# Performance work log

Measured on AMD Instinct MI355X. Metric: run time of the kernel, lower is better.

Reference implementation:

```python
import jax, jax.numpy as jnp
import numpy as np

NUM_ITER = 3
SLOT_DIM = 16
INPUT_DIM = 256
HIDDEN_DIM = 128
EPS = 1e-8
LN_EPS = 1e-5  # torch LayerNorm default


def _layernorm(x, w, b):
    mu = jnp.mean(x, axis=-1, keepdims=True)
    var = jnp.mean((x - mu) ** 2, axis=-1, keepdims=True)
    return (x - mu) * jax.lax.rsqrt(var + LN_EPS) * w + b


def setup_inputs() -> dict:
    key = jax.random.key(0)
    ks = jax.random.split(key, 12)
    B, N, K = 32, 4096, 8
    D, S, H = INPUT_DIM, SLOT_DIM, HIDDEN_DIM
    inputs = jax.random.normal(ks[0], (B, N, D), dtype=jnp.float32)
    init_slots = jax.random.normal(ks[1], (B, K, S), dtype=jnp.float32)
    return {
        "inputs": inputs,
        "init_slots": init_slots,
        "ln_in_w": jnp.ones((D,), jnp.float32),
        "ln_in_b": jnp.zeros((D,), jnp.float32),
        "ln_s_w": jnp.ones((S,), jnp.float32),
        "ln_s_b": jnp.zeros((S,), jnp.float32),
        "ln_m_w": jnp.ones((S,), jnp.float32),
        "ln_m_b": jnp.zeros((S,), jnp.float32),
        "wq": jax.random.normal(ks[2], (S, S), jnp.float32) * (S ** -0.5),
        "wk": jax.random.normal(ks[3], (S, D), jnp.float32) * (D ** -0.5),
        "wv": jax.random.normal(ks[4], (S, D), jnp.float32) * (D ** -0.5),
        "w_ih": jax.random.normal(ks[5], (3 * S, S), jnp.float32) * (S ** -0.5),
        "w_hh": jax.random.normal(ks[6], (3 * S, S), jnp.float32) * (S ** -0.5),
        "b_ih": jnp.zeros((3 * S,), jnp.float32),
        "b_hh": jnp.zeros((3 * S,), jnp.float32),
        "mlp_w1": jax.random.normal(ks[7], (H, S), jnp.float32) * (S ** -0.5),
        "mlp_b1": jnp.zeros((H,), jnp.float32),
        "mlp_w2": jax.random.normal(ks[8], (S, H), jnp.float32) * (H ** -0.5),
        "mlp_b2": jnp.zeros((S,), jnp.float32),
    }


def _gru_cell(x, h, w_ih, w_hh, b_ih, b_hh):
    # torch GRUCell: gates ordered [r, z, n]
    gi = x @ w_ih.T + b_ih            # [BK, 3S]
    gh = h @ w_hh.T + b_hh
    i_r, i_z, i_n = jnp.split(gi, 3, axis=-1)
    h_r, h_z, h_n = jnp.split(gh, 3, axis=-1)
    r = jax.nn.sigmoid(i_r + h_r)
    z = jax.nn.sigmoid(i_z + h_z)
    n = jnp.tanh(i_n + r * h_n)
    return (1.0 - z) * n + z * h


def reference(inputs, init_slots, ln_in_w, ln_in_b, ln_s_w, ln_s_b, ln_m_w, ln_m_b,
              wq, wk, wv, w_ih, w_hh, b_ih, b_hh, mlp_w1, mlp_b1, mlp_w2, mlp_b2):
    B, N, _ = inputs.shape
    K = init_slots.shape[1]
    scale = SLOT_DIM ** -0.5

    x = _layernorm(inputs, ln_in_w, ln_in_b)
    k = jnp.einsum('bnd,sd->bns', x, wk)   # [B,N,S]
    v = jnp.einsum('bnd,sd->bns', x, wv)

    slots = init_slots
    attn = None
    for _ in range(NUM_ITER):
        slots_prev = slots
        q = jnp.einsum('bks,ts->bkt', _layernorm(slots, ln_s_w, ln_s_b), wq)
        logits = jnp.einsum('bks,bns->bkn', q, k) * scale       # [B,K,N]
        attn = jax.nn.softmax(logits, axis=1) + EPS              # softmax over SLOTS
        attn = attn / jnp.sum(attn, axis=-1, keepdims=True)
        updates = jnp.einsum('bkn,bns->bks', attn, v)            # [B,K,S]
        h = _gru_cell(updates.reshape(B * K, -1), slots_prev.reshape(B * K, -1),
                      w_ih, w_hh, b_ih, b_hh).reshape(B, K, -1)
        y = _layernorm(h, ln_m_w, ln_m_b)
        mlp = jax.nn.relu(y @ mlp_w1.T + mlp_b1) @ mlp_w2.T + mlp_b2
        slots = h + mlp
    return slots, attn
```

## Files before the change

### kernel.cpp

```cpp
#include <hip/hip_runtime.h>
#include <cstddef>


typedef unsigned short ushort_t;
typedef __attribute__((ext_vector_type(8))) short short8;
typedef __attribute__((ext_vector_type(4))) float f32x4;

__device__ __forceinline__ float sigmoid_f(float x){ return 1.f/(1.f+__expf(-x)); }
__device__ __forceinline__ float tanh_f(float x){ return 1.f - 2.f/(__expf(2.f*x)+1.f); }

__device__ __forceinline__ ushort_t f2bf(float x){
  unsigned u = __float_as_uint(x);
  return (ushort_t)((u + 0x7FFFu + ((u>>16)&1u)) >> 16);
}
__device__ __forceinline__ float bf2f(ushort_t b){
  return __uint_as_float(((unsigned)b) << 16);
}
__device__ __forceinline__ void split_bf(float v, short& hi, short& lo){
  unsigned u = __float_as_uint(v);
  hi = (short)(u >> 16);
  float hf = __uint_as_float(u & 0xFFFF0000u);
  lo = (short)(__float_as_uint(v - hf) >> 16);
}

__global__ __launch_bounds__(256) void k_prep(
    const float* __restrict__ lnw, const float* __restrict__ lnb,
    const float* __restrict__ wk, const float* __restrict__ wv,
    const float* __restrict__ init_slots,
    const float* __restrict__ ln_s_w, const float* __restrict__ ln_s_b,
    const float* __restrict__ wq,
    ushort_t* __restrict__ Wh, ushort_t* __restrict__ Wl,
    float* __restrict__ mt,
    float* __restrict__ qbuf, float* __restrict__ upd, float* __restrict__ Abuf,
    float* __restrict__ slots_out)
{
  int t = threadIdx.x;
  int i = blockIdx.x*256 + t;
  {
    int s = i >> 8, d = i & 255;
    float w = (s < 16) ? wk[s*256+d] : wv[(s-16)*256+d];
    float w0 = lnw[d]*w;
    ushort_t hb = f2bf(w0);
    ushort_t lb = f2bf(w0 - bf2f(hb));
    Wh[i] = hb; Wl[i] = lb;
  }
  if (blockIdx.x != 0) return;
  {
    int s = t >> 3, j = t & 7;
    float m = 0.f, tv = 0.f;
    for (int d = j; d < 256; d += 8) {
      float w = (s < 16) ? wk[s*256+d] : wv[(s-16)*256+d];
      float w0 = lnw[d]*w;
      ushort_t hb = f2bf(w0);
      float hf = bf2f(hb);
      float lf = bf2f(f2bf(w0 - hf));
      m  += hf + lf;
      tv  = fmaf(lnb[d], w, tv);
    }
    m += __shfl_xor(m,1);  m += __shfl_xor(m,2);  m += __shfl_xor(m,4);
    tv += __shfl_xor(tv,1); tv += __shfl_xor(tv,2); tv += __shfl_xor(tv,4);
    if (j == 0) { mt[s] = m; mt[32+s] = tv; }
  }
  #pragma unroll
  for (int j2 = 0; j2 < 16; ++j2) {
    slots_out[t*16+j2] = init_slots[t*16+j2];
    upd[t*16+j2] = 0.f;
  }
  Abuf[t] = 0.f;
  float sl[16];
  #pragma unroll
  for (int j2 = 0; j2 < 16; ++j2) sl[j2] = init_slots[t*16+j2];
  float mu = 0.f;
  #pragma unroll
  for (int j2 = 0; j2 < 16; ++j2) mu += sl[j2];
  mu *= (1.f/16.f);
  float var = 0.f;
  #pragma unroll
  for (int j2 = 0; j2 < 16; ++j2) { float d = sl[j2]-mu; var = fmaf(d,d,var); }
  var *= (1.f/16.f);
  float rstd = rsqrtf(var + 1e-5f);
  float y[16];
  #pragma unroll
  for (int j2 = 0; j2 < 16; ++j2) y[j2] = (sl[j2]-mu)*rstd*ln_s_w[j2] + ln_s_b[j2];
  #pragma unroll
  for (int tq = 0; tq < 16; ++tq) {
    float q = 0.f;
    #pragma unroll
    for (int s2 = 0; s2 < 16; ++s2) q = fmaf(y[s2], wq[tq*16+s2], q);
    qbuf[t*16+tq] = q;
  }
}

__global__ __launch_bounds__(256, 4) void k_proj(
    const float* __restrict__ x, const ushort_t* __restrict__ Wh,
    const ushort_t* __restrict__ Wl, const float* __restrict__ mt,
    float* __restrict__ kout, float* __restrict__ vout)
{
  __shared__ ushort_t wlds[64*264];
  int t = threadIdx.x;
  int lane = t & 63;
  int p = __builtin_amdgcn_readfirstlane(t >> 6);
  int m = lane & 15, quad = lane >> 4;
  int r0 = blockIdx.x*64;

  {
    const unsigned* srcH = (const unsigned*)Wh;
    const unsigned* srcL = (const unsigned*)Wl;
    unsigned* dst = (unsigned*)wlds;
    #pragma unroll
    for (int i0 = 0; i0 < 8192; i0 += 256) {
      int i = i0 + t;
      int r = i >> 7, w = i & 127;
      unsigned v = (r < 32) ? srcH[r*128 + w] : srcL[(r-32)*128 + w];
      dst[r*132 + w] = v;
    }
  }
  __syncthreads();

  const ushort_t* rhk = wlds + (size_t)m*264 + quad*8;
  const ushort_t* rhv = wlds + (size_t)(16+m)*264 + quad*8;
  const ushort_t* rlk = wlds + (size_t)(32+m)*264 + quad*8;
  const ushort_t* rlv = wlds + (size_t)(48+m)*264 + quad*8;

  const float* xr = x + (size_t)(r0 + p*16 + m)*256 + quad*8;

  f32x4 acck = {0.f,0.f,0.f,0.f}, accv = {0.f,0.f,0.f,0.f};
  float sum = 0.f, sumsq = 0.f;

  #pragma unroll
  for (int kk = 0; kk < 8; ++kk) {
    float4 a0 = *(const float4*)(xr + kk*32);
    float4 a1 = *(const float4*)(xr + kk*32 + 4);
    short8 bh_k = *(const short8*)(rhk + kk*32);
    short8 bh_v = *(const short8*)(rhv + kk*32);
    short8 bl_k = *(const short8*)(rlk + kk*32);
    short8 bl_v = *(const short8*)(rlv + kk*32);
    float xv[8] = {a0.x,a0.y,a0.z,a0.w, a1.x,a1.y,a1.z,a1.w};
    short8 ah, al;
    #pragma unroll
    for (int j = 0; j < 8; ++j) {
      float v = xv[j];
      sum += v; sumsq = fmaf(v, v, sumsq);
      short h_, l_;
      split_bf(v, h_, l_);
      ah[j] = h_; al[j] = l_;
    }
    acck = __builtin_amdgcn_mfma_f32_16x16x32_bf16(ah, bh_k, acck, 0, 0, 0);
    accv = __builtin_amdgcn_mfma_f32_16x16x32_bf16(ah, bh_v, accv, 0, 0, 0);
    acck = __builtin_amdgcn_mfma_f32_16x16x32_bf16(al, bh_k, acck, 0, 0, 0);
    accv = __builtin_amdgcn_mfma_f32_16x16x32_bf16(al, bh_v, accv, 0, 0, 0);
    acck = __builtin_amdgcn_mfma_f32_16x16x32_bf16(ah, bl_k, acck, 0, 0, 0);
    accv = __builtin_amdgcn_mfma_f32_16x16x32_bf16(ah, bl_v, accv, 0, 0, 0);
  }

  sum   += __shfl_xor(sum, 16);  sum   += __shfl_xor(sum, 32);
  sumsq += __shfl_xor(sumsq, 16); sumsq += __shfl_xor(sumsq, 32);

  float mtk  = mt[m],    mtv  = mt[16+m];
  float mtkb = mt[32+m], mtvb = mt[48+m];
  #pragma unroll
  for (int r = 0; r < 4; ++r) {
    int row = quad*4 + r;
    float s_ = __shfl(sum,   row);
    float q_ = __shfl(sumsq, row);
    float mu = s_*(1.f/256.f);
    float var = q_*(1.f/256.f) - mu*mu;
    float rstd = rsqrtf(var + 1e-5f);
    float ok = fmaf(rstd, acck[r] - mu*mtk, mtkb);
    float ov = fmaf(rstd, accv[r] - mu*mtv, mtvb);
    size_t grow = (size_t)(r0 + p*16 + row)*16 + m;
    kout[grow] = ok;
    vout[grow] = ov;
  }
}

__global__ __launch_bounds__(256) void k_attn(
    const float* __restrict__ kproj, const float* __restrict__ vproj,
    const float* __restrict__ qbuf,
    float* __restrict__ upd, float* __restrict__ Abuf,
    float* __restrict__ attn_out, int write_attn)
{
  __shared__ ushort_t vt[32*264];
  __shared__ ushort_t pt[32*264];
  __shared__ float qs[128];
  __shared__ float apart[4][8];
  int b = blockIdx.x >> 4;
  int n0 = (blockIdx.x & 15) * 256;
  int t = threadIdx.x;
  int w = t >> 6, lane = t & 63;

  if (t < 128) qs[t] = qbuf[b*128 + t];

  const float* kr = kproj + ((size_t)(b*4096 + n0 + t))*16;
  const float* vr = vproj + ((size_t)(b*4096 + n0 + t))*16;
  float kv[16], vv[16];
  #pragma unroll
  for (int j = 0; j < 16; j += 4) {
    float4 f = *(const float4*)(kr+j);
    kv[j]=f.x; kv[j+1]=f.y; kv[j+2]=f.z; kv[j+3]=f.w;
    float4 g = *(const float4*)(vr+j);
    vv[j]=g.x; vv[j+1]=g.y; vv[j+2]=g.z; vv[j+3]=g.w;
  }
  #pragma unroll
  for (int s = 0; s < 16; ++s) {
    short h_, l_;
    split_bf(vv[s], h_, l_);
    vt[s*264 + t] = (ushort_t)h_;
    vt[(16+s)*264 + t] = (ushort_t)l_;
  }
  __syncthreads();

  float p8[8];
  {
    float lg[8];
    #pragma unroll
    for (int kk = 0; kk < 8; ++kk) {
      float a = 0.f;
      #pragma unroll
      for (int s = 0; s < 16; ++s) a = fmaf(qs[kk*16+s], kv[s], a);
      lg[kk] = a*0.25f;
    }
    float mx = lg[0];
    #pragma unroll
    for (int kk = 1; kk < 8; ++kk) mx = fmaxf(mx, lg[kk]);
    float se = 0.f;
    #pragma unroll
    for (int kk = 0; kk < 8; ++kk) { lg[kk] = __expf(lg[kk]-mx); se += lg[kk]; }
    float inv = 1.f/se;
    #pragma unroll
    for (int kk = 0; kk < 8; ++kk) {
      float pv = fmaf(lg[kk], inv, 1e-8f);
      p8[kk] = pv;
      if (write_attn) attn_out[((size_t)(b*8+kk))*4096 + n0 + t] = pv;
    }
  }
  #pragma unroll
  for (int kk = 0; kk < 8; ++kk) {
    float r = p8[kk];
    r += __shfl_xor(r, 1);  r += __shfl_xor(r, 2);  r += __shfl_xor(r, 4);
    r += __shfl_xor(r, 8);  r += __shfl_xor(r, 16); r += __shfl_xor(r, 32);
    if (lane == 0) apart[w][kk] = r;
  }
  #pragma unroll
  for (int kk = 0; kk < 8; ++kk) {
    short h_, l_;
    split_bf(p8[kk], h_, l_);
    pt[kk*264 + t] = (ushort_t)h_;
    pt[(16+kk)*264 + t] = (ushort_t)l_;
  }
  __syncthreads();

  if (t < 8)
    atomicAdd(Abuf + b*8 + t,
              apart[0][t] + apart[1][t] + apart[2][t] + apart[3][t]);

  if (w == 0) {
    int mm = lane & 15, quad = lane >> 4;
    const short8 z8 = {0,0,0,0,0,0,0,0};
    f32x4 acc = {0.f,0.f,0.f,0.f};
    #pragma unroll
    for (int c = 0; c < 8; ++c) {
      int k0 = c*32 + quad*8;
      short8 ah = (mm < 8) ? *(const short8*)&pt[mm*264 + k0]      : z8;
      short8 al = (mm < 8) ? *(const short8*)&pt[(16+mm)*264 + k0] : z8;
      short8 bh = *(const short8*)&vt[mm*264 + k0];
      short8 bl = *(const short8*)&vt[(16+mm)*264 + k0];
      acc = __builtin_amdgcn_mfma_f32_16x16x32_bf16(ah, bh, acc, 0, 0, 0);
      acc = __builtin_amdgcn_mfma_f32_16x16x32_bf16(al, bh, acc, 0, 0, 0);
      acc = __builtin_amdgcn_mfma_f32_16x16x32_bf16(ah, bl, acc, 0, 0, 0);
    }
    int s = lane & 15;
    #pragma unroll
    for (int r = 0; r < 4; ++r) {
      int kk = quad*4 + r;
      if (kk < 8) atomicAdd(upd + (b*8+kk)*16 + s, acc[r]);
    }
  }
}

__device__ __forceinline__ void gru_body(
    int bk, int s, int laneBase, int prep_next,
    float* upd, float* Abuf, float* slots, float* qbuf,
    const float* s_wih, const float* s_whh,
    const float* s_bih, const float* s_bhh,
    const float* s_w1, const float* s_b1,
    const float* s_w2, const float* s_b2,
    const float* s_lnmw, const float* s_lnmb,
    const float* s_lnsw, const float* s_lnsb, const float* s_wq)
{
  float inv = 1.f / Abuf[bk];
  float u[16], h[16];
  #pragma unroll
  for (int j = 0; j < 16; ++j) {
    u[j] = upd[bk*16+j] * inv;
    h[j] = slots[bk*16+j];
  }
  float hs = slots[bk*16+s];

  float gir = s_bih[s],  giz = s_bih[16+s], gin = s_bih[32+s];
  float ghr = s_bhh[s],  ghz = s_bhh[16+s], ghn = s_bhh[32+s];
  #pragma unroll
  for (int j = 0; j < 16; ++j) {
    gir = fmaf(u[j], s_wih[s*17+j], gir);
    giz = fmaf(u[j], s_wih[(16+s)*17+j], giz);
    gin = fmaf(u[j], s_wih[(32+s)*17+j], gin);
    ghr = fmaf(h[j], s_whh[s*17+j], ghr);
    ghz = fmaf(h[j], s_whh[(16+s)*17+j], ghz);
    ghn = fmaf(h[j], s_whh[(32+s)*17+j], ghn);
  }
  float rr = sigmoid_f(gir + ghr);
  float zz = sigmoid_f(giz + ghz);
  float nn = tanh_f(gin + rr*ghn);
  float hn = (1.f-zz)*nn + zz*hs;

  float ssum = hn;
  #pragma unroll
  for (int mm = 1; mm < 16; mm <<= 1) ssum += __shfl_xor(ssum, mm);
  float mu = ssum*(1.f/16.f);
  float dv = hn - mu;
  float vs = dv*dv;
  #pragma unroll
  for (int mm = 1; mm < 16; mm <<= 1) vs += __shfl_xor(vs, mm);
  float rstd = rsqrtf(vs*(1.f/16.f) + 1e-5f);
  float y = dv*rstd*s_lnmw[s] + s_lnmb[s];

  float yv[16];
  #pragma unroll
  for (int j = 0; j < 16; ++j) yv[j] = __shfl(y, laneBase + j);

  float h1[8];
  #pragma unroll
  for (int i = 0; i < 8; ++i) {
    int jj = i*16 + s;
    float a = s_b1[jj];
    #pragma unroll
    for (int q = 0; q < 16; ++q) a = fmaf(yv[q], s_w1[jj*17+q], a);
    h1[i] = fmaxf(a, 0.f);
  }
  float o = s_b2[s];
  #pragma unroll
  for (int i = 0; i < 8; ++i) {
    #pragma unroll
    for (int sp = 0; sp < 16; ++sp) {
      float hv = __shfl(h1[i], laneBase + sp);
      o = fmaf(hv, s_w2[s*129 + i*16 + sp], o);
    }
  }
  float slot_new = hn + o;
  slots[bk*16+s] = slot_new;

  if (prep_next) {
    float ss = slot_new;
    #pragma unroll
    for (int mm = 1; mm < 16; mm <<= 1) ss += __shfl_xor(ss, mm);
    float mu2 = ss*(1.f/16.f);
    float d2 = slot_new - mu2;
    float v2 = d2*d2;
    #pragma unroll
    for (int mm = 1; mm < 16; mm <<= 1) v2 += __shfl_xor(v2, mm);
    float rstd2 = rsqrtf(v2*(1.f/16.f) + 1e-5f);
    float y2 = d2*rstd2*s_lnsw[s] + s_lnsb[s];
    float qv = 0.f;
    #pragma unroll
    for (int sp = 0; sp < 16; ++sp)
      qv = fmaf(__shfl(y2, laneBase+sp), s_wq[s*17+sp], qv);
    qbuf[bk*16+s] = qv;
    upd[bk*16+s] = 0.f;
    if (s == 0) Abuf[bk] = 0.f;
  }
}

#define GRU_STAGE_LDS()                                                      \
  __shared__ float s_wih[48*17], s_whh[48*17];                               \
  __shared__ float s_bih[48], s_bhh[48];                                     \
  __shared__ float s_w1[128*17], s_b1[128];                                  \
  __shared__ float s_w2[16*129], s_b2[16];                                   \
  __shared__ float s_lnmw[16], s_lnmb[16], s_lnsw[16], s_lnsb[16];           \
  __shared__ float s_wq[16*17];                                              \
  {                                                                          \
    int t_ = threadIdx.x;                                                    \
    for (int i = t_; i < 768; i += 256) {                                    \
      int g = i >> 4, j = i & 15;                                            \
      s_wih[g*17+j] = w_ih[i];                                               \
      s_whh[g*17+j] = w_hh[i];                                               \
    }                                                                        \
    for (int i = t_; i < 2048; i += 256) {                                   \
      int r = i >> 4, c = i & 15;                                            \
      s_w1[r*17+c] = mlp_w1[i];                                              \
      int r2 = i >> 7, c2 = i & 127;                                         \
      s_w2[r2*129+c2] = mlp_w2[i];                                           \
    }                                                                        \
    if (t_ < 48) { s_bih[t_] = b_ih[t_]; s_bhh[t_] = b_hh[t_]; }             \
    if (t_ < 128) s_b1[t_] = mlp_b1[t_];                                     \
    if (t_ < 16) {                                                           \
      s_b2[t_] = mlp_b2[t_];                                                 \
      s_lnmw[t_] = ln_m_w[t_]; s_lnmb[t_] = ln_m_b[t_];                      \
      s_lnsw[t_] = ln_s_w[t_]; s_lnsb[t_] = ln_s_b[t_];                      \
    }                                                                        \
    for (int i = t_; i < 256; i += 256) {                                    \
      int r = i >> 4, c = i & 15;                                            \
      s_wq[r*17+c] = wq[i];                                                  \
    }                                                                        \
  }                                                                          \
  __syncthreads();

__global__ __launch_bounds__(256) void k_gru(
    float* __restrict__ upd, float* __restrict__ Abuf,
    float* __restrict__ slots, float* __restrict__ qbuf,
    const float* __restrict__ w_ih, const float* __restrict__ w_hh,
    const float* __restrict__ b_ih, const float* __restrict__ b_hh,
    const float* __restrict__ mlp_w1, const float* __restrict__ mlp_b1,
    const float* __restrict__ mlp_w2, const float* __restrict__ mlp_b2,
    const float* __restrict__ ln_m_w, const float* __restrict__ ln_m_b,
    const float* __restrict__ ln_s_w, const float* __restrict__ ln_s_b,
    const float* __restrict__ wq)
{
  GRU_STAGE_LDS()
  int t = threadIdx.x;
  int bk = blockIdx.x*16 + (t >> 4);
  int s = t & 15;
  int laneBase = (t & 63) & ~15;
  gru_body(bk, s, laneBase, 1, upd, Abuf, slots, qbuf,
           s_wih, s_whh, s_bih, s_bhh, s_w1, s_b1, s_w2, s_b2,
           s_lnmw, s_lnmb, s_lnsw, s_lnsb, s_wq);
}

__global__ __launch_bounds__(256) void k_final(
    float* __restrict__ upd, float* __restrict__ Abuf,
    float* __restrict__ slots, float* __restrict__ qbuf,
    float* __restrict__ attn,
    const float* __restrict__ w_ih, const float* __restrict__ w_hh,
    const float* __restrict__ b_ih, const float* __restrict__ b_hh,
    const float* __restrict__ mlp_w1, const float* __restrict__ mlp_b1,
    const float* __restrict__ mlp_w2, const float* __restrict__ mlp_b2,
    const float* __restrict__ ln_m_w, const float* __restrict__ ln_m_b,
    const float* __restrict__ ln_s_w, const float* __restrict__ ln_s_b,
    const float* __restrict__ wq)
{
  int t = threadIdx.x;
  {
    int bk = blockIdx.x;
    float inv = 1.f / Abuf[bk];
    float4* p = (float4*)(attn + (size_t)bk*4096);
    #pragma unroll 4
    for (int i = t; i < 1024; i += 256) {
      float4 v = p[i];
      v.x *= inv; v.y *= inv; v.z *= inv; v.w *= inv;
      p[i] = v;
    }
  }
  if (blockIdx.x >= 16) return;
  GRU_STAGE_LDS()
  int bk = blockIdx.x*16 + (t >> 4);
  int s = t & 15;
  int laneBase = (t & 63) & ~15;
  gru_body(bk, s, laneBase, 0, upd, Abuf, slots, qbuf,
           s_wih, s_whh, s_bih, s_bhh, s_w1, s_b1, s_w2, s_b2,
           s_lnmw, s_lnmb, s_lnsw, s_lnsb, s_wq);
}

extern "C" void kernel_launch(void* const* d_in, const int* in_sizes, int n_in,
                              void* d_out, int out_size, void* d_ws, size_t ws_size,
                              hipStream_t stream)
{
  const float* inputs     = (const float*)d_in[0];
  const float* init_slots = (const float*)d_in[1];
  const float* ln_in_w    = (const float*)d_in[2];
  const float* ln_in_b    = (const float*)d_in[3];
  const float* ln_s_w     = (const float*)d_in[4];
  const float* ln_s_b     = (const float*)d_in[5];
  const float* ln_m_w     = (const float*)d_in[6];
  const float* ln_m_b     = (const float*)d_in[7];
  const float* wq         = (const float*)d_in[8];
  const float* wk         = (const float*)d_in[9];
  const float* wv         = (const float*)d_in[10];
  const float* w_ih       = (const float*)d_in[11];
  const float* w_hh       = (const float*)d_in[12];
  const float* b_ih       = (const float*)d_in[13];
  const float* b_hh       = (const float*)d_in[14];
  const float* mlp_w1     = (const float*)d_in[15];
  const float* mlp_b1     = (const float*)d_in[16];
  const float* mlp_w2     = (const float*)d_in[17];
  const float* mlp_b2     = (const float*)d_in[18];

  float* ws    = (float*)d_ws;
  ushort_t* Wh = (ushort_t*)ws;
  ushort_t* Wl = (ushort_t*)(ws + 4096);
  float* mt    = ws + 8192;
  float* qbuf  = ws + 8320;
  float* upd   = ws + 12416;
  float* Abuf  = ws + 16512;
  float* kproj = ws + 16768;
  float* vproj = kproj + 2097152;

  float* out   = (float*)d_out;
  float* slots = out;
  float* attn  = out + 4096;

  k_prep<<<32, 256, 0, stream>>>(ln_in_w, ln_in_b, wk, wv, init_slots,
                                 ln_s_w, ln_s_b, wq,
                                 Wh, Wl, mt, qbuf, upd, Abuf, slots);
  k_proj<<<2048, 256, 0, stream>>>(inputs, Wh, Wl, mt, kproj, vproj);
  for (int it = 0; it < 3; ++it) {
    int last = (it == 2);
    k_attn<<<512, 256, 0, stream>>>(kproj, vproj, qbuf, upd, Abuf, attn, last);
    if (!last)
      k_gru<<<16, 256, 0, stream>>>(upd, Abuf, slots, qbuf,
                                    w_ih, w_hh, b_ih, b_hh,
                                    mlp_w1, mlp_b1, mlp_w2, mlp_b2,
                                    ln_m_w, ln_m_b, ln_s_w, ln_s_b, wq);
  }
  k_final<<<256, 256, 0, stream>>>(upd, Abuf, slots, qbuf, attn,
                                   w_ih, w_hh, b_ih, b_hh,
                                   mlp_w1, mlp_b1, mlp_w2, mlp_b2,
                                   ln_m_w, ln_m_b, ln_s_w, ln_s_b, wq);
}
```

Baseline: 287.2 us.

## Fuse projection, attention iterations and GRU into one cooperative kernel

```diff
diff --git a/kernel.cpp b/kernel.cpp
--- a/kernel.cpp
+++ b/kernel.cpp
@@ -1,5 +1,8 @@
 #include <hip/hip_runtime.h>
+#include <hip/hip_cooperative_groups.h>
 #include <cstddef>
+
+namespace cg = cooperative_groups;
 
 
 typedef unsigned short ushort_t;
@@ -62,11 +65,10 @@
     if (j == 0) { mt[s] = m; mt[32+s] = tv; }
   }
   #pragma unroll
-  for (int j2 = 0; j2 < 16; ++j2) {
+  for (int j2 = 0; j2 < 16; ++j2)
     slots_out[t*16+j2] = init_slots[t*16+j2];
-    upd[t*16+j2] = 0.f;
-  }
-  Abuf[t] = 0.f;
+  for (int i2 = t; i2 < 12288; i2 += 256) upd[i2] = 0.f;
+  for (int i2 = t; i2 < 768;   i2 += 256) Abuf[i2] = 0.f;
   float sl[16];
   #pragma unroll
   for (int j2 = 0; j2 < 16; ++j2) sl[j2] = init_slots[t*16+j2];
@@ -90,6 +92,337 @@
     qbuf[t*16+tq] = q;
   }
 }
+
+#define VT_OFF    0
+#define QS_OFF    16896
+#define SLOTS_OFF 17408
+#define APART_OFF 17920
+#define X_OFF     18048
+#define KLDS_OFF  (X_OFF + 33792)
+#define PT_OFF    X_OFF
+#define GW_OFF    (X_OFF + 8448)
+#define SMEM_BYTES 60544
+
+__global__ __launch_bounds__(256, 2) void k_mega(
+    const float* __restrict__ x,
+    const ushort_t* __restrict__ Wh, const ushort_t* __restrict__ Wl,
+    const float* __restrict__ mt, const float* __restrict__ qbuf,
+    const float* __restrict__ init_slots,
+    float* __restrict__ upd, float* __restrict__ Abuf,
+    float* __restrict__ slots_out, float* __restrict__ attn_out,
+    const float* __restrict__ w_ih, const float* __restrict__ w_hh,
+    const float* __restrict__ b_ih, const float* __restrict__ b_hh,
+    const float* __restrict__ mlp_w1, const float* __restrict__ mlp_b1,
+    const float* __restrict__ mlp_w2, const float* __restrict__ mlp_b2,
+    const float* __restrict__ ln_m_w, const float* __restrict__ ln_m_b,
+    const float* __restrict__ ln_s_w, const float* __restrict__ ln_s_b,
+    const float* __restrict__ wq)
+{
+  cg::grid_group grid = cg::this_grid();
+  __shared__ __align__(16) unsigned char smem[SMEM_BYTES];
+  ushort_t* vt     = (ushort_t*)(smem + VT_OFF);
+  float*    qs     = (float*)(smem + QS_OFF);
+  float*    sslots = (float*)(smem + SLOTS_OFF);
+  float*    apart  = (float*)(smem + APART_OFF);
+  ushort_t* wlds   = (ushort_t*)(smem + X_OFF);
+  float*    klds   = (float*)(smem + KLDS_OFF);
+  ushort_t* pt     = (ushort_t*)(smem + PT_OFF);
+  float*    s_wih  = (float*)(smem + GW_OFF);
+  float*    s_whh  = s_wih + 48*17;
+  float*    s_w1   = s_whh + 48*17;
+  float*    s_w2   = s_w1 + 128*17;
+  float*    s_bih  = s_w2 + 16*129;
+  float*    s_bhh  = s_bih + 48;
+  float*    s_b1   = s_bhh + 48;
+  float*    s_b2   = s_b1 + 128;
+  float*    s_lnmw = s_b2 + 16;
+  float*    s_lnmb = s_lnmw + 16;
+  float*    s_lnsw = s_lnmb + 16;
+  float*    s_lnsb = s_lnsw + 16;
+  float*    s_wq   = s_lnsb + 16;
+
+  int t = threadIdx.x;
+  int lane = t & 63;
+  int w = t >> 6;
+  int b  = blockIdx.x >> 4;
+  int nc = blockIdx.x & 15;
+  int n0 = nc << 8;
+
+  {
+    const unsigned* srcH = (const unsigned*)Wh;
+    const unsigned* srcL = (const unsigned*)Wl;
+    unsigned* dst = (unsigned*)wlds;
+    #pragma unroll
+    for (int i0 = 0; i0 < 8192; i0 += 256) {
+      int i = i0 + t;
+      int r = i >> 7, ww = i & 127;
+      unsigned v = (r < 32) ? srcH[r*128 + ww] : srcL[(r-32)*128 + ww];
+      dst[r*132 + ww] = v;
+    }
+  }
+  __syncthreads();
+
+  int m = lane & 15, quad = lane >> 4;
+  const ushort_t* rhk = wlds + (size_t)m*264 + quad*8;
+  const ushort_t* rhv = wlds + (size_t)(16+m)*264 + quad*8;
+  const ushort_t* rlk = wlds + (size_t)(32+m)*264 + quad*8;
+  const ushort_t* rlv = wlds + (size_t)(48+m)*264 + quad*8;
+  float mtk  = mt[m],    mtv  = mt[16+m];
+  float mtkb = mt[32+m], mtvb = mt[48+m];
+
+  float kv[16] = {0.f};
+  #pragma unroll
+  for (int half = 0; half < 2; ++half) {
+    #pragma unroll
+    for (int st = 0; st < 2; ++st) {
+      const float* xr = x + (size_t)(b*4096 + n0 + half*128 + st*64 + w*16 + m)*256
+                          + quad*8;
+      f32x4 acck = {0.f,0.f,0.f,0.f}, accv = {0.f,0.f,0.f,0.f};
+      float sum = 0.f, sumsq = 0.f;
+      #pragma unroll
+      for (int kk = 0; kk < 8; ++kk) {
+        float4 a0 = *(const float4*)(xr + kk*32);
+        float4 a1 = *(const float4*)(xr + kk*32 + 4);
+        short8 bh_k = *(const short8*)(rhk + kk*32);
+        short8 bh_v = *(const short8*)(rhv + kk*32);
+        short8 bl_k = *(const short8*)(rlk + kk*32);
+        short8 bl_v = *(const short8*)(rlv + kk*32);
+        float xv[8] = {a0.x,a0.y,a0.z,a0.w, a1.x,a1.y,a1.z,a1.w};
+        short8 ah, al;
+        #pragma unroll
+        for (int j = 0; j < 8; ++j) {
+          float v = xv[j];
+          sum += v; sumsq = fmaf(v, v, sumsq);
+          short h_, l_;
+          split_bf(v, h_, l_);
+          ah[j] = h_; al[j] = l_;
+        }
+        acck = __builtin_amdgcn_mfma_f32_16x16x32_bf16(ah, bh_k, acck, 0, 0, 0);
+        accv = __builtin_amdgcn_mfma_f32_16x16x32_bf16(ah, bh_v, accv, 0, 0, 0);
+        acck = __builtin_amdgcn_mfma_f32_16x16x32_bf16(al, bh_k, acck, 0, 0, 0);
+        accv = __builtin_amdgcn_mfma_f32_16x16x32_bf16(al, bh_v, accv, 0, 0, 0);
+        acck = __builtin_amdgcn_mfma_f32_16x16x32_bf16(ah, bl_k, acck, 0, 0, 0);
+        accv = __builtin_amdgcn_mfma_f32_16x16x32_bf16(ah, bl_v, accv, 0, 0, 0);
+      }
+      sum   += __shfl_xor(sum, 16);   sum   += __shfl_xor(sum, 32);
+      sumsq += __shfl_xor(sumsq, 16); sumsq += __shfl_xor(sumsq, 32);
+      #pragma unroll
+      for (int r = 0; r < 4; ++r) {
+        int row = quad*4 + r;
+        float s_ = __shfl(sum,   row);
+        float q_ = __shfl(sumsq, row);
+        float mu = s_*(1.f/256.f);
+        float var = q_*(1.f/256.f) - mu*mu;
+        float rstd = rsqrtf(var + 1e-5f);
+        float ok = fmaf(rstd, acck[r] - mu*mtk, mtkb);
+        float ov = fmaf(rstd, accv[r] - mu*mtv, mtvb);
+        int lr = st*64 + w*16 + row;
+        int rr = half*128 + lr;
+        klds[lr*17 + m] = ok;
+        short h_, l_;
+        split_bf(ov, h_, l_);
+        vt[m*264 + rr]      = (ushort_t)h_;
+        vt[(16+m)*264 + rr] = (ushort_t)l_;
+      }
+    }
+    __syncthreads();
+    if ((t >> 7) == half) {
+      int tl = t & 127;
+      #pragma unroll
+      for (int j = 0; j < 16; ++j) kv[j] = klds[tl*17 + j];
+    }
+    __syncthreads();
+  }
+
+  for (int i = t; i < 768; i += 256) {
+    int g = i >> 4, j = i & 15;
+    s_wih[g*17+j] = w_ih[i];
+    s_whh[g*17+j] = w_hh[i];
+  }
+  for (int i = t; i < 2048; i += 256) {
+    int r = i >> 4, c = i & 15;
+    s_w1[r*17+c] = mlp_w1[i];
+    int r2 = i >> 7, c2 = i & 127;
+    s_w2[r2*129+c2] = mlp_w2[i];
+  }
+  if (t < 48) { s_bih[t] = b_ih[t]; s_bhh[t] = b_hh[t]; }
+  if (t < 128) s_b1[t] = mlp_b1[t];
+  if (t < 16) {
+    s_b2[t] = mlp_b2[t];
+    s_lnmw[t] = ln_m_w[t]; s_lnmb[t] = ln_m_b[t];
+    s_lnsw[t] = ln_s_w[t]; s_lnsb[t] = ln_s_b[t];
+  }
+  for (int i = t; i < 256; i += 256) {
+    int r = i >> 4, c = i & 15;
+    s_wq[r*17+c] = wq[i];
+  }
+  if (t < 128) {
+    qs[t]     = qbuf[b*128 + t];
+    sslots[t] = init_slots[b*128 + t];
+  }
+  __syncthreads();
+
+  const short8 z8 = {0,0,0,0,0,0,0,0};
+  #pragma unroll 1
+  for (int it = 0; it < 3; ++it) {
+    float* upd_it = upd  + it*4096;
+    float* Ab_it  = Abuf + it*256;
+
+    float p8[8];
+    {
+      float lg[8];
+      #pragma unroll
+      for (int kk = 0; kk < 8; ++kk) {
+        float a = 0.f;
+        #pragma unroll
+        for (int s = 0; s < 16; ++s) a = fmaf(qs[kk*16+s], kv[s], a);
+        lg[kk] = a*0.25f;
+      }
+      float mx = lg[0];
+      #pragma unroll
+      for (int kk = 1; kk < 8; ++kk) mx = fmaxf(mx, lg[kk]);
+      float se = 0.f;
+      #pragma unroll
+      for (int kk = 0; kk < 8; ++kk) { lg[kk] = __expf(lg[kk]-mx); se += lg[kk]; }
+      float inv = 1.f/se;
+      #pragma unroll
+      for (int kk = 0; kk < 8; ++kk) p8[kk] = fmaf(lg[kk], inv, 1e-8f);
+    }
+    #pragma unroll
+    for (int kk = 0; kk < 8; ++kk) {
+      float r = p8[kk];
+      r += __shfl_xor(r, 1);  r += __shfl_xor(r, 2);  r += __shfl_xor(r, 4);
+      r += __shfl_xor(r, 8);  r += __shfl_xor(r, 16); r += __shfl_xor(r, 32);
+      if (lane == 0) apart[w*8 + kk] = r;
+    }
+    #pragma unroll
+    for (int kk = 0; kk < 8; ++kk) {
+      short h_, l_;
+      split_bf(p8[kk], h_, l_);
+      pt[kk*264 + t]     = (ushort_t)h_;
+      pt[(8+kk)*264 + t] = (ushort_t)l_;
+    }
+    __syncthreads();
+    if (t < 8)
+      atomicAdd(Ab_it + b*8 + t,
+                apart[t] + apart[8+t] + apart[16+t] + apart[24+t]);
+    if (w == 0) {
+      int mm = lane & 15, q2 = lane >> 4;
+      f32x4 acc = {0.f,0.f,0.f,0.f};
+      #pragma unroll
+      for (int c = 0; c < 8; ++c) {
+        int k0 = c*32 + q2*8;
+        short8 ah = (mm < 8) ? *(const short8*)&pt[mm*264 + k0]     : z8;
+        short8 al = (mm < 8) ? *(const short8*)&pt[(8+mm)*264 + k0] : z8;
+        short8 bh = *(const short8*)&vt[mm*264 + k0];
+        short8 bl = *(const short8*)&vt[(16+mm)*264 + k0];
+        acc = __builtin_amdgcn_mfma_f32_16x16x32_bf16(ah, bh, acc, 0, 0, 0);
+        acc = __builtin_amdgcn_mfma_f32_16x16x32_bf16(al, bh, acc, 0, 0, 0);
+        acc = __builtin_amdgcn_mfma_f32_16x16x32_bf16(ah, bl, acc, 0, 0, 0);
+      }
+      int s = lane & 15;
+      #pragma unroll
+      for (int r = 0; r < 4; ++r) {
+        int kk = q2*4 + r;
+        if (kk < 8) atomicAdd(upd_it + (b*8+kk)*16 + s, acc[r]);
+      }
+    }
+    __threadfence();
+    grid.sync();
+
+    if (it == 2) {
+      #pragma unroll
+      for (int kk = 0; kk < 8; ++kk) {
+        float inv = 1.f / Ab_it[b*8 + kk];
+        attn_out[((size_t)(b*8 + kk))*4096 + n0 + t] = p8[kk]*inv;
+      }
+    }
+    if (t < 128) {
+      int bk8 = t >> 4, s = t & 15;
+      int laneBase = (t & 63) & ~15;
+      float invA = 1.f / Ab_it[b*8 + bk8];
+      float u[16], h[16];
+      #pragma unroll
+      for (int j = 0; j < 16; ++j) {
+        u[j] = upd_it[(b*8 + bk8)*16 + j] * invA;
+        h[j] = sslots[bk8*16 + j];
+      }
+      float hs = h[s];
+      float gir = s_bih[s],  giz = s_bih[16+s], gin = s_bih[32+s];
+      float ghr = s_bhh[s],  ghz = s_bhh[16+s], ghn = s_bhh[32+s];
+      #pragma unroll
+      for (int j = 0; j < 16; ++j) {
+        gir = fmaf(u[j], s_wih[s*17+j], gir);
+        giz = fmaf(u[j], s_wih[(16+s)*17+j], giz);
+        gin = fmaf(u[j], s_wih[(32+s)*17+j], gin);
+        ghr = fmaf(h[j], s_whh[s*17+j], ghr);
+        ghz = fmaf(h[j], s_whh[(16+s)*17+j], ghz);
+        ghn = fmaf(h[j], s_whh[(32+s)*17+j], ghn);
+      }
+      float rr_ = sigmoid_f(gir + ghr);
+      float zz = sigmoid_f(giz + ghz);
+      float nn = tanh_f(gin + rr_*ghn);
+      float hn = (1.f - zz)*nn + zz*hs;
+
+      float ssum = hn;
+      #pragma unroll
+      for (int mm = 1; mm < 16; mm <<= 1) ssum += __shfl_xor(ssum, mm);
+      float mu = ssum*(1.f/16.f);
+      float dv = hn - mu;
+      float vs = dv*dv;
+      #pragma unroll
+      for (int mm = 1; mm < 16; mm <<= 1) vs += __shfl_xor(vs, mm);
+      float rstd = rsqrtf(vs*(1.f/16.f) + 1e-5f);
+      float y = dv*rstd*s_lnmw[s] + s_lnmb[s];
+
+      float yv[16];
+      #pragma unroll
+      for (int j = 0; j < 16; ++j) yv[j] = __shfl(y, laneBase + j);
+
+      float h1[8];
+      #pragma unroll
+      for (int i = 0; i < 8; ++i) {
+        int jj = i*16 + s;
+        float a = s_b1[jj];
+        #pragma unroll
+        for (int q = 0; q < 16; ++q) a = fmaf(yv[q], s_w1[jj*17+q], a);
+        h1[i] = fmaxf(a, 0.f);
+      }
+      float o = s_b2[s];
+      #pragma unroll
+      for (int i = 0; i < 8; ++i) {
+        #pragma unroll
+        for (int sp = 0; sp < 16; ++sp) {
+          float hv = __shfl(h1[i], laneBase + sp);
+          o = fmaf(hv, s_w2[s*129 + i*16 + sp], o);
+        }
+      }
+      float slot_new = hn + o;
+      if (it < 2) {
+        sslots[bk8*16 + s] = slot_new;
+        float ss = slot_new;
+        #pragma unroll
+        for (int mm = 1; mm < 16; mm <<= 1) ss += __shfl_xor(ss, mm);
+        float mu2 = ss*(1.f/16.f);
+        float d2 = slot_new - mu2;
+        float v2 = d2*d2;
+        #pragma unroll
+        for (int mm = 1; mm < 16; mm <<= 1) v2 += __shfl_xor(v2, mm);
+        float rstd2 = rsqrtf(v2*(1.f/16.f) + 1e-5f);
+        float y2 = d2*rstd2*s_lnsw[s] + s_lnsb[s];
+        float qv = 0.f;
+        #pragma unroll
+        for (int sp = 0; sp < 16; ++sp)
+          qv = fmaf(__shfl(y2, laneBase + sp), s_wq[s*17+sp], qv);
+        qs[bk8*16 + s] = qv;
+      } else if (nc == 0) {
+        slots_out[(b*8 + bk8)*16 + s] = slot_new;
+      }
+    }
+    __syncthreads();
+  }
+}
+
 
 __global__ __launch_bounds__(256, 4) void k_proj(
     const float* __restrict__ x, const ushort_t* __restrict__ Wh,
@@ -102,7 +435,6 @@
   int p = __builtin_amdgcn_readfirstlane(t >> 6);
   int m = lane & 15, quad = lane >> 4;
   int r0 = blockIdx.x*64;
-
   {
     const unsigned* srcH = (const unsigned*)Wh;
     const unsigned* srcL = (const unsigned*)Wl;
@@ -489,8 +821,8 @@
   float* mt    = ws + 8192;
   float* qbuf  = ws + 8320;
   float* upd   = ws + 12416;
-  float* Abuf  = ws + 16512;
-  float* kproj = ws + 16768;
+  float* Abuf  = ws + 24704;
+  float* kproj = ws + 25472;
   float* vproj = kproj + 2097152;
 
   float* out   = (float*)d_out;
@@ -500,6 +832,22 @@
   k_prep<<<32, 256, 0, stream>>>(ln_in_w, ln_in_b, wk, wv, init_slots,
                                  ln_s_w, ln_s_b, wq,
                                  Wh, Wl, mt, qbuf, upd, Abuf, slots);
+
+  {
+    void* kargs[] = {
+      (void*)&inputs, (void*)&Wh, (void*)&Wl, (void*)&mt, (void*)&qbuf,
+      (void*)&init_slots, (void*)&upd, (void*)&Abuf, (void*)&slots,
+      (void*)&attn, (void*)&w_ih, (void*)&w_hh, (void*)&b_ih, (void*)&b_hh,
+      (void*)&mlp_w1, (void*)&mlp_b1, (void*)&mlp_w2, (void*)&mlp_b2,
+      (void*)&ln_m_w, (void*)&ln_m_b, (void*)&ln_s_w, (void*)&ln_s_b,
+      (void*)&wq };
+    hipError_t err = hipLaunchCooperativeKernel((const void*)k_mega,
+                                                dim3(512), dim3(256),
+                                                kargs, 0, stream);
+    if (err == hipSuccess) return;
+    (void)hipGetLastError();
+  }
+
   k_proj<<<2048, 256, 0, stream>>>(inputs, Wh, Wl, mt, kproj, vproj);
   for (int it = 0; it < 3; ++it) {
     int last = (it == 2);
```

New measurement: 563.0 us. 96.1% more time.

## Store V pre-split to bf16 hi/lo planes transposed in projection kernel

Applied to the files above, without the earlier changes.

```diff
diff --git a/kernel.cpp b/kernel.cpp
--- a/kernel.cpp
+++ b/kernel.cpp
@@ -5,6 +5,8 @@
 typedef unsigned short ushort_t;
 typedef __attribute__((ext_vector_type(8))) short short8;
 typedef __attribute__((ext_vector_type(4))) float f32x4;
+
+#define VT_PLANE 2097152
 
 __device__ __forceinline__ float sigmoid_f(float x){ return 1.f/(1.f+__expf(-x)); }
 __device__ __forceinline__ float tanh_f(float x){ return 1.f - 2.f/(__expf(2.f*x)+1.f); }
@@ -94,15 +96,15 @@
 __global__ __launch_bounds__(256, 4) void k_proj(
     const float* __restrict__ x, const ushort_t* __restrict__ Wh,
     const ushort_t* __restrict__ Wl, const float* __restrict__ mt,
-    float* __restrict__ kout, float* __restrict__ vout)
+    float* __restrict__ kout, ushort_t* __restrict__ vT)
 {
   __shared__ ushort_t wlds[64*264];
+  __shared__ ushort_t vtile[2*1024];
   int t = threadIdx.x;
   int lane = t & 63;
   int p = __builtin_amdgcn_readfirstlane(t >> 6);
   int m = lane & 15, quad = lane >> 4;
   int r0 = blockIdx.x*64;
-
   {
     const unsigned* srcH = (const unsigned*)Wh;
     const unsigned* srcL = (const unsigned*)Wl;
@@ -168,20 +170,32 @@
     float rstd = rsqrtf(var + 1e-5f);
     float ok = fmaf(rstd, acck[r] - mu*mtk, mtkb);
     float ov = fmaf(rstd, accv[r] - mu*mtv, mtvb);
-    size_t grow = (size_t)(r0 + p*16 + row)*16 + m;
-    kout[grow] = ok;
-    vout[grow] = ov;
+    int lrow = p*16 + row;
+    kout[(size_t)(r0 + lrow)*16 + m] = ok;
+    short h_, l_;
+    split_bf(ov, h_, l_);
+    vtile[m*64 + lrow]        = (ushort_t)h_;
+    vtile[1024 + m*64 + lrow] = (ushort_t)l_;
+  }
+  __syncthreads();
+  {
+    int plane = t >> 7;
+    int idx   = t & 127;
+    int s = idx >> 3;
+    int b = r0 >> 12, nbase = r0 & 4095;
+    short8 v8 = *(const short8*)&vtile[plane*1024 + idx*8];
+    *(short8*)&vT[(size_t)plane*VT_PLANE + ((size_t)(b*16 + s))*4096
+                  + nbase + (idx & 7)*8] = v8;
   }
 }
 
 __global__ __launch_bounds__(256) void k_attn(
-    const float* __restrict__ kproj, const float* __restrict__ vproj,
+    const float* __restrict__ kproj, const ushort_t* __restrict__ vT,
     const float* __restrict__ qbuf,
     float* __restrict__ upd, float* __restrict__ Abuf,
     float* __restrict__ attn_out, int write_attn)
 {
-  __shared__ ushort_t vt[32*264];
-  __shared__ ushort_t pt[32*264];
+  __shared__ ushort_t pt[16*264];
   __shared__ float qs[128];
   __shared__ float apart[4][8];
   int b = blockIdx.x >> 4;
@@ -192,21 +206,11 @@
   if (t < 128) qs[t] = qbuf[b*128 + t];
 
   const float* kr = kproj + ((size_t)(b*4096 + n0 + t))*16;
-  const float* vr = vproj + ((size_t)(b*4096 + n0 + t))*16;
-  float kv[16], vv[16];
+  float kv[16];
   #pragma unroll
   for (int j = 0; j < 16; j += 4) {
     float4 f = *(const float4*)(kr+j);
     kv[j]=f.x; kv[j+1]=f.y; kv[j+2]=f.z; kv[j+3]=f.w;
-    float4 g = *(const float4*)(vr+j);
-    vv[j]=g.x; vv[j+1]=g.y; vv[j+2]=g.z; vv[j+3]=g.w;
-  }
-  #pragma unroll
-  for (int s = 0; s < 16; ++s) {
-    short h_, l_;
-    split_bf(vv[s], h_, l_);
-    vt[s*264 + t] = (ushort_t)h_;
-    vt[(16+s)*264 + t] = (ushort_t)l_;
   }
   __syncthreads();
 
@@ -245,8 +249,8 @@
   for (int kk = 0; kk < 8; ++kk) {
     short h_, l_;
     split_bf(p8[kk], h_, l_);
-    pt[kk*264 + t] = (ushort_t)h_;
-    pt[(16+kk)*264 + t] = (ushort_t)l_;
+    pt[kk*264 + t]     = (ushort_t)h_;
+    pt[(8+kk)*264 + t] = (ushort_t)l_;
   }
   __syncthreads();
 
@@ -257,14 +261,16 @@
   if (w == 0) {
     int mm = lane & 15, quad = lane >> 4;
     const short8 z8 = {0,0,0,0,0,0,0,0};
+    const ushort_t* vhi = vT + ((size_t)(b*16 + mm))*4096 + n0;
+    const ushort_t* vlo = vhi + (size_t)VT_PLANE;
     f32x4 acc = {0.f,0.f,0.f,0.f};
     #pragma unroll
     for (int c = 0; c < 8; ++c) {
       int k0 = c*32 + quad*8;
-      short8 ah = (mm < 8) ? *(const short8*)&pt[mm*264 + k0]      : z8;
-      short8 al = (mm < 8) ? *(const short8*)&pt[(16+mm)*264 + k0] : z8;
-      short8 bh = *(const short8*)&vt[mm*264 + k0];
-      short8 bl = *(const short8*)&vt[(16+mm)*264 + k0];
+      short8 ah = (mm < 8) ? *(const short8*)&pt[mm*264 + k0]     : z8;
+      short8 al = (mm < 8) ? *(const short8*)&pt[(8+mm)*264 + k0] : z8;
+      short8 bh = *(const short8*)(vhi + k0);
+      short8 bl = *(const short8*)(vlo + k0);
       acc = __builtin_amdgcn_mfma_f32_16x16x32_bf16(ah, bh, acc, 0, 0, 0);
       acc = __builtin_amdgcn_mfma_f32_16x16x32_bf16(al, bh, acc, 0, 0, 0);
       acc = __builtin_amdgcn_mfma_f32_16x16x32_bf16(ah, bl, acc, 0, 0, 0);
@@ -491,7 +497,7 @@
   float* upd   = ws + 12416;
   float* Abuf  = ws + 16512;
   float* kproj = ws + 16768;
-  float* vproj = kproj + 2097152;
+  ushort_t* vT = (ushort_t*)(ws + 16768 + 2097152);
 
   float* out   = (float*)d_out;
   float* slots = out;
@@ -500,10 +506,10 @@
   k_prep<<<32, 256, 0, stream>>>(ln_in_w, ln_in_b, wk, wv, init_slots,
                                  ln_s_w, ln_s_b, wq,
                                  Wh, Wl, mt, qbuf, upd, Abuf, slots);
-  k_proj<<<2048, 256, 0, stream>>>(inputs, Wh, Wl, mt, kproj, vproj);
+  k_proj<<<2048, 256, 0, stream>>>(inputs, Wh, Wl, mt, kproj, vT);
   for (int it = 0; it < 3; ++it) {
     int last = (it == 2);
-    k_attn<<<512, 256, 0, stream>>>(kproj, vproj, qbuf, upd, Abuf, attn, last);
+    k_attn<<<512, 256, 0, stream>>>(kproj, vT, qbuf, upd, Abuf, attn, last);
     if (!last)
       k_gru<<<16, 256, 0, stream>>>(upd, Abuf, slots, qbuf,
                                     w_ih, w_hh, b_ih, b_hh,
```

Measured after the change: 290.6 us. Within noise of the previous version (+1.2%).
